# Optimization experiments

Hardware: AMD Instinct MI355X
Metric: run time of the kernel (lower is better)

Reference implementation:

```python
import jax, jax.numpy as jnp
import numpy as np

N, R, A, F = 6000, 5, 8, 128
K, O = 2, 128
RADIUS = 0.028
ROT_DELTA = 1


def _kernel_matrix(n_radial, n_angular, radius):
    # polar grid of kernel vertices -> cartesian, shape (R, A, 2)
    r = radius * (np.arange(1, n_radial + 1, dtype=np.float64) / n_radial)
    theta = 2.0 * np.pi * np.arange(n_angular, dtype=np.float64) / n_angular
    x = r[:, None] * np.cos(theta)[None, :]
    y = r[:, None] * np.sin(theta)[None, :]
    return np.stack([x, y], axis=-1)


def _interp_coefficients(n_radial, n_angular, radius):
    # Gaussian interpolation weights w(rho_a,theta_b,rho_c,theta_d), normalized,
    # reshaped to (R, A, R*A) as in _configure_patch_operator.
    kv = _kernel_matrix(n_radial, n_angular, radius)           # (R, A, 2)
    flat = kv.reshape(-1, 2)                                   # (R*A, 2)
    d2 = ((kv[:, :, None, :] - flat[None, None, :, :]) ** 2).sum(-1)  # (R, A, R*A)
    sigma = radius / n_radial
    w = np.exp(-d2 / (2.0 * sigma * sigma))
    w = w / w.sum(axis=-1, keepdims=True)
    return w.astype(np.float32)


def setup_inputs() -> dict:
    key = jax.random.key(0)
    k1, k2, k3, k4, k5 = jax.random.split(key, 5)
    mesh_signal = jax.random.normal(k1, (N, F), dtype=jnp.float32)
    # barycentric coords: channel 0 = vertex indices (stored as float), channel 1 = weights summing to 1
    idx = jax.random.randint(k2, (N, R, A, 3), 0, N).astype(jnp.float32)
    w = jax.random.uniform(k3, (N, R, A, 3), dtype=jnp.float32)
    w = w / w.sum(axis=-1, keepdims=True)
    bary_coordinates = jnp.stack([idx, w], axis=-1)            # (N, R, A, 3, 2)
    kernel_weights = jax.random.normal(k4, (R, A, K, O, F), dtype=jnp.float32) * 0.05
    bias = jax.random.normal(k5, (K, O), dtype=jnp.float32) * 0.05
    interp_coeffs = jnp.asarray(_interp_coefficients(R, A, RADIUS))  # (R, A, R*A)
    return {"mesh_signal": mesh_signal, "bary_coordinates": bary_coordinates,
            "kernel_weights": kernel_weights, "bias": bias, "interp_coeffs": interp_coeffs}


def reference(mesh_signal, bary_coordinates, kernel_weights, bias, interp_coeffs):
    # 1) gather + barycentric interpolation
    idx = bary_coordinates[..., 0].astype(jnp.int32)           # (N, R, A, 3)
    w = bary_coordinates[..., 1]                               # (N, R, A, 3)
    collected = mesh_signal[idx]                               # (N, R, A, 3, F)
    sig = jnp.sum(w[..., None] * collected, axis=-2)           # (N, R, A, F)
    # 2) patch operator: F_x @ I[a,b]
    flat = sig.reshape(-1, R * A, F)                           # (N, R*A, F)
    patched = jnp.einsum('nqf,raq->nraf', flat, interp_coeffs)  # (N, R, A, F)
    # 3) rotation-shifted fold (splits=1 -> single chunk; splits don't change math)
    outs = []
    for rot in range(0, A, ROT_DELTA):
        rolled = jnp.roll(patched, shift=rot, axis=2)          # (N, R, A, F)
        s = jnp.einsum('nraf,rakof->nko', rolled, kernel_weights) + (R * A) * bias  # (N, K, O)
        outs.append(jax.nn.relu(s).sum(axis=1))                # (N, O)
    return jnp.stack(outs, axis=1)                             # (N, n_rotations, O)
```

## Files before the change

kernel.cpp:

```cpp
#include <hip/hip_runtime.h>
#include <hip/hip_bf16.h>


#define N_PTS 6000
#define RR 5
#define AA 8
#define FF 128
#define OO 128
#define QQ 40
#define KD2 1280
#define SIG_BLOCKS 750
#define W2_BLOCKS 128
#define CCQ 0.70710678118654752f
#define RT2 1.41421356237309515f

#define AHS ((size_t)N_PTS * KD2)
#define BHS ((size_t)512 * KD2)

typedef __bf16 bf16_t;
typedef __bf16 bf16x4 __attribute__((ext_vector_type(4)));
typedef __bf16 bf16x8 __attribute__((ext_vector_type(8)));
typedef float f32x4 __attribute__((ext_vector_type(4)));

#define GLOAD_LDS16(g, l)                                              \
  __builtin_amdgcn_global_load_lds(                                    \
      (const __attribute__((address_space(1))) void*)(g),              \
      (__attribute__((address_space(3))) void*)(l), 16, 0, 0)

#define DFT8V(xx, c, X0, X4, Xr1, Xi1, Xr2, Xi2, Xr3, Xi3)             \
  {                                                                    \
    const float s0_ = xx[0][c] + xx[4][c], s1_ = xx[1][c] + xx[5][c];  \
    const float s2_ = xx[2][c] + xx[6][c], s3_ = xx[3][c] + xx[7][c];  \
    const float d0_ = xx[0][c] - xx[4][c], d1_ = xx[1][c] - xx[5][c];  \
    const float d2_ = xx[2][c] - xx[6][c], d3_ = xx[3][c] - xx[7][c];  \
    const float e_ = CCQ * (d1_ - d3_), o_ = CCQ * (d1_ + d3_);        \
    X0 = (s0_ + s2_) + (s1_ + s3_);                                    \
    X4 = (s0_ + s2_) - (s1_ + s3_);                                    \
    Xr2 = s0_ - s2_; Xi2 = s3_ - s1_;                                  \
    Xr1 = d0_ + e_;  Xi1 = -(o_ + d2_);                                \
    Xr3 = d0_ - e_;  Xi3 = d2_ - o_;                                   \
  }

#define PACK4(dst, X)                                                  \
  {                                                                    \
    bf16x4 pv_;                                                        \
    pv_[0] = (bf16_t)X[0]; pv_[1] = (bf16_t)X[1];                      \
    pv_[2] = (bf16_t)X[2]; pv_[3] = (bf16_t)X[3];                      \
    *(bf16x4*)(dst) = pv_;                                             \
  }

__global__ __launch_bounds__(256) void prep_fft_kernel(
    const float* __restrict__ mesh, const float* __restrict__ bary,
    const float* __restrict__ kw, const float* __restrict__ interp,
    bf16_t* __restrict__ Ahat, bf16_t* __restrict__ Bhat) {
  __shared__ float sI[RR * AA * QQ];
  const int bx = blockIdx.x;
  const int tid = threadIdx.x;

  if (bx < SIG_BLOCKS) {
    const int slot = tid >> 5;
    const int l = tid & 31;
    const int n = bx * 8 + slot;
    const float* bn = bary + (size_t)n * (QQ * 6);
    bf16_t* an = Ahat + (size_t)n * KD2 + l * 4;
#pragma unroll
    for (int rho = 0; rho < RR; ++rho) {
      float x[8][4];
#pragma unroll
      for (int a = 0; a < 8; ++a) {
        const float* b = bn + (rho * 8 + a) * 6;
        const float2 p0 = *(const float2*)(b);
        const float2 p1 = *(const float2*)(b + 2);
        const float2 p2 = *(const float2*)(b + 4);
        const float4 v0 =
            *(const float4*)(mesh + (size_t)((int)p0.x) * FF + l * 4);
        const float4 v1 =
            *(const float4*)(mesh + (size_t)((int)p1.x) * FF + l * 4);
        const float4 v2 =
            *(const float4*)(mesh + (size_t)((int)p2.x) * FF + l * 4);
        x[a][0] = p0.y * v0.x + p1.y * v1.x + p2.y * v2.x;
        x[a][1] = p0.y * v0.y + p1.y * v1.y + p2.y * v2.y;
        x[a][2] = p0.y * v0.z + p1.y * v1.z + p2.y * v2.z;
        x[a][3] = p0.y * v0.w + p1.y * v1.w + p2.y * v2.w;
      }
      float X0[4], X4[4], Xr1[4], Xi1[4], Xr2[4], Xi2[4], Xr3[4], Xi3[4];
#pragma unroll
      for (int c = 0; c < 4; ++c)
        DFT8V(x, c, X0[c], X4[c], Xr1[c], Xi1[c], Xr2[c], Xi2[c], Xr3[c],
              Xi3[c]);
      bf16_t* dst = an + rho * 256;
      PACK4(dst, X0);                  PACK4(dst + 128, X4);
      PACK4(dst + AHS, Xr1);           PACK4(dst + AHS + 128, Xi1);
      PACK4(dst + 2 * AHS, Xr2);       PACK4(dst + 2 * AHS + 128, Xi2);
      PACK4(dst + 3 * AHS, Xr3);       PACK4(dst + 3 * AHS + 128, Xi3);
    }
  } else {
    const int j = (bx - SIG_BLOCKS) * 2 + (tid >> 7);
    const int f = tid & 127;
    for (int i = tid; i < RR * AA * QQ; i += 256) sI[i] = interp[i];
    __syncthreads();
    const int o = (j >> 1) & 127;
    const int k = j & 1;
    float acc[QQ];
#pragma unroll
    for (int q = 0; q < QQ; ++q) acc[q] = 0.f;
    for (int r = 0; r < RR; ++r) {
      for (int a = 0; a < AA; ++a) {
        const float kv =
            kw[((size_t)((r * AA + a) * 2 + k) * OO + o) * FF + f];
        const float4* ip = (const float4*)(sI + (r * AA + a) * QQ);
#pragma unroll
        for (int q4 = 0; q4 < QQ / 4; ++q4) {
          const float4 w4 = ip[q4];
          acc[q4 * 4 + 0] += w4.x * kv;
          acc[q4 * 4 + 1] += w4.y * kv;
          acc[q4 * 4 + 2] += w4.z * kv;
          acc[q4 * 4 + 3] += w4.w * kv;
        }
      }
    }
    const float SC = 0.125f;
    bf16_t* b1p = Bhat + (size_t)j * KD2 + f;
    bf16_t* b2p = Bhat + (size_t)(256 + j) * KD2 + f;
#pragma unroll
    for (int rho = 0; rho < RR; ++rho) {
      float xx[8][1];
#pragma unroll
      for (int a = 0; a < 8; ++a) xx[a][0] = acc[rho * 8 + a];
      float Y0, Y4, Yr1, Yi1, Yr2, Yi2, Yr3, Yi3;
      DFT8V(xx, 0, Y0, Y4, Yr1, Yi1, Yr2, Yi2, Yr3, Yi3);
      const int off = rho * 256;
      b1p[off] = (bf16_t)(Y0 * SC);        b1p[off + 128] = (bf16_t)0.f;
      b2p[off] = (bf16_t)0.f;              b2p[off + 128] = (bf16_t)(Y4 * SC);
      b1p[BHS + off] = (bf16_t)(Yr1 * SC);
      b1p[BHS + off + 128] = (bf16_t)(Yi1 * SC);
      b2p[BHS + off] = (bf16_t)(Yi1 * SC);
      b2p[BHS + off + 128] = (bf16_t)(-Yr1 * SC);
      b1p[2 * BHS + off] = (bf16_t)(Yr2 * SC);
      b1p[2 * BHS + off + 128] = (bf16_t)(Yi2 * SC);
      b2p[2 * BHS + off] = (bf16_t)(Yi2 * SC);
      b2p[2 * BHS + off + 128] = (bf16_t)(-Yr2 * SC);
      b1p[3 * BHS + off] = (bf16_t)(Yr3 * SC);
      b1p[3 * BHS + off + 128] = (bf16_t)(Yi3 * SC);
      b2p[3 * BHS + off] = (bf16_t)(Yi3 * SC);
      b2p[3 * BHS + off + 128] = (bf16_t)(-Yr3 * SC);
    }
  }
}

__global__ __launch_bounds__(256, 3) void gemm_fused_fft_kernel(
    const bf16_t* __restrict__ Ahat, const bf16_t* __restrict__ Bhat,
    const float* __restrict__ bias, float* __restrict__ out) {
  const int L = blockIdx.x;
  const int xcd = L & 7;
  const int t = L >> 3;
  const int g = xcd + 8 * (t >> 4);
  const int jt = t & 15;
  const int m0 = g * 128;
  if (m0 >= N_PTS) return;
  const int j0 = jt * 16;

  __shared__ bf16_t As[128 * 64];
  __shared__ bf16_t Bs[32 * 64];
  const int tid = threadIdx.x;
  const int wave = tid >> 6;
  const int lane = tid & 63;
  const int quad = lane >> 4;
  const int tl = lane & 15;
  const int wm = wave * 32;
  const int srow = lane >> 3;
  const int sc = (lane & 7) ^ srow;

  const int crow = wave * 8;
  const int colbase = (crow < 16) ? (j0 + crow) : (256 + j0 + (crow - 16));
  const int gcol = colbase + srow;

  static const float CF[4][8] = {
      {1, 1, 1, 1, 1, 1, 1, 1},
      {2, RT2, 0, -RT2, -2, -RT2, 0, RT2},
      {2, 0, -2, 0, 2, 0, -2, 0},
      {2, -RT2, 0, RT2, -2, RT2, 0, -RT2}};
  static const float SF[4][8] = {
      {1, -1, 1, -1, 1, -1, 1, -1},
      {0, -RT2, -2, -RT2, 0, RT2, 2, RT2},
      {0, -2, 0, 2, 0, -2, 0, 2},
      {0, -RT2, 2, -RT2, 0, RT2, -2, RT2}};

  f32x4 oacc[8][2];
#pragma unroll
  for (int rot = 0; rot < 8; ++rot)
#pragma unroll
    for (int mm = 0; mm < 2; ++mm) oacc[rot][mm] = {0.f, 0.f, 0.f, 0.f};

#pragma unroll
  for (int b = 0; b < 4; ++b) {
    const bf16_t* A = Ahat + (size_t)b * AHS;
    const bf16_t* B = Bhat + (size_t)b * BHS;
    f32x4 z[2][2];
#pragma unroll
    for (int mm = 0; mm < 2; ++mm)
#pragma unroll
      for (int cc = 0; cc < 2; ++cc) z[mm][cc] = {0.f, 0.f, 0.f, 0.f};

    for (int kk = 0; kk < KD2; kk += 64) {
      __syncthreads();
#pragma unroll
      for (int i = 0; i < 4; ++i) {
        const int row = wave * 32 + i * 8;
        int gm = m0 + row + srow;
        gm = gm < N_PTS ? gm : (N_PTS - 1);
        GLOAD_LDS16(A + (size_t)gm * KD2 + kk + sc * 8, As + row * 64);
      }
      GLOAD_LDS16(B + (size_t)gcol * KD2 + kk + sc * 8, Bs + crow * 64);
      __syncthreads();
#pragma unroll
      for (int ks = 0; ks < 2; ++ks) {
        const int ch = (((ks * 4 + quad) ^ (tl & 7)) * 8);
        bf16x8 af[2], bfr[2];
        af[0] = *(const bf16x8*)(As + (wm + tl) * 64 + ch);
        af[1] = *(const bf16x8*)(As + (wm + 16 + tl) * 64 + ch);
        bfr[0] = *(const bf16x8*)(Bs + tl * 64 + ch);
        bfr[1] = *(const bf16x8*)(Bs + (16 + tl) * 64 + ch);
#pragma unroll
        for (int mm = 0; mm < 2; ++mm)
#pragma unroll
          for (int cc = 0; cc < 2; ++cc)
            z[mm][cc] = __builtin_amdgcn_mfma_f32_16x16x32_bf16(
                af[mm], bfr[cc], z[mm][cc], 0, 0, 0);
      }
    }
#pragma unroll
    for (int rot = 0; rot < 8; ++rot) {
      const float cf = CF[b][rot], sf = SF[b][rot];
#pragma unroll
      for (int mm = 0; mm < 2; ++mm)
#pragma unroll
        for (int r = 0; r < 4; ++r)
          oacc[rot][mm][r] += cf * z[mm][0][r] + sf * z[mm][1][r];
    }
  }

  const int j = j0 + tl;
  const float bb = 40.0f * bias[((j & 1) << 7) | (j >> 1)];
  const int o = j >> 1;
#pragma unroll
  for (int rot = 0; rot < 8; ++rot)
#pragma unroll
    for (int mm = 0; mm < 2; ++mm)
#pragma unroll
      for (int r = 0; r < 4; ++r) {
        const int mrow = m0 + wm + mm * 16 + quad * 4 + r;
        float v = oacc[rot][mm][r] + bb;
        v = v > 0.f ? v : 0.f;
        const float vs = v + __shfl_xor(v, 1, 64);
        if (((lane & 1) == 0) && (mrow < N_PTS))
          out[(size_t)mrow * 1024 + rot * 128 + o] = vs;
      }
}

extern "C" void kernel_launch(void* const* d_in, const int* in_sizes, int n_in,
                              void* d_out, int out_size, void* d_ws,
                              size_t ws_size, hipStream_t stream) {
  const float* mesh = (const float*)d_in[0];
  const float* bary = (const float*)d_in[1];
  const float* kw = (const float*)d_in[2];
  const float* bias = (const float*)d_in[3];
  const float* interp = (const float*)d_in[4];
  float* out = (float*)d_out;

  bf16_t* Ahat = (bf16_t*)d_ws;
  bf16_t* Bhat = (bf16_t*)((char*)d_ws + 4 * AHS * 2);

  prep_fft_kernel<<<SIG_BLOCKS + W2_BLOCKS, 256, 0, stream>>>(
      mesh, bary, kw, interp, Ahat, Bhat);
  gemm_fused_fft_kernel<<<768, 256, 0, stream>>>(Ahat, Bhat, bias, out);
}
```

Baseline: 160.3 us.

## Double-buffer B tiles in LDS and load A fragments directly into registers

Restructures the GEMM main loop into a software pipeline. B tiles are staged through two alternating LDS buffers, and the A operand is loaded straight from global memory into MFMA register fragments instead of going through shared memory. The next tile's loads, including the first tile of the next FFT component, are issued before computing on the current one, which halves the barriers per tile and overlaps memory latency with MFMA work. In exchange it uses more registers for the prefetched A fragments. The A loads also lose coalescing, since each lane now reads 16-byte chunks from separate rows.

Result: slower. 229.4 us (+43.1%).

```diff
diff --git a/kernel.cpp b/kernel.cpp
--- a/kernel.cpp
+++ b/kernel.cpp
@@ -160,8 +160,8 @@
   if (m0 >= N_PTS) return;
   const int j0 = jt * 16;
 
-  __shared__ bf16_t As[128 * 64];
-  __shared__ bf16_t Bs[32 * 64];
+  __shared__ bf16_t Bs0[32 * 64];
+  __shared__ bf16_t Bs1[32 * 64];
   const int tid = threadIdx.x;
   const int wave = tid >> 6;
   const int lane = tid & 63;
@@ -173,7 +173,12 @@
 
   const int crow = wave * 8;
   const int colbase = (crow < 16) ? (j0 + crow) : (256 + j0 + (crow - 16));
-  const int gcol = colbase + srow;
+  const size_t bcol = (size_t)(colbase + srow) * KD2 + sc * 8;
+
+  int r0 = m0 + wm + tl;       r0 = r0 < N_PTS ? r0 : (N_PTS - 1);
+  int r1 = m0 + wm + 16 + tl;  r1 = r1 < N_PTS ? r1 : (N_PTS - 1);
+  const size_t ro0 = (size_t)r0 * KD2 + quad * 8;
+  const size_t ro1 = (size_t)r1 * KD2 + quad * 8;
 
   static const float CF[4][8] = {
       {1, 1, 1, 1, 1, 1, 1, 1},
@@ -192,52 +197,82 @@
 #pragma unroll
     for (int mm = 0; mm < 2; ++mm) oacc[rot][mm] = {0.f, 0.f, 0.f, 0.f};
 
+#define STAGE_B(Bp, kkv, bufn) \
+  GLOAD_LDS16((Bp) + bcol + (kkv), Bs##bufn + crow * 64)
+
+#define LOAD_A(p0, p1, p2, p3, Ap, kkv)                   \
+  p0 = *(const bf16x8*)((Ap) + ro0 + (kkv));              \
+  p1 = *(const bf16x8*)((Ap) + ro1 + (kkv));              \
+  p2 = *(const bf16x8*)((Ap) + ro0 + (kkv) + 32);         \
+  p3 = *(const bf16x8*)((Ap) + ro1 + (kkv) + 32);
+
+#define COMPUTE(Bsx, p0, p1, p2, p3)                                        \
+  {                                                                         \
+    const int ch0 = (quad ^ (tl & 7)) * 8;                                  \
+    const int ch1 = ((4 + quad) ^ (tl & 7)) * 8;                            \
+    bf16x8 b0 = *(const bf16x8*)(Bsx + tl * 64 + ch0);                      \
+    bf16x8 b1 = *(const bf16x8*)(Bsx + (16 + tl) * 64 + ch0);               \
+    z00 = __builtin_amdgcn_mfma_f32_16x16x32_bf16(p0, b0, z00, 0, 0, 0);    \
+    z01 = __builtin_amdgcn_mfma_f32_16x16x32_bf16(p0, b1, z01, 0, 0, 0);    \
+    z10 = __builtin_amdgcn_mfma_f32_16x16x32_bf16(p1, b0, z10, 0, 0, 0);    \
+    z11 = __builtin_amdgcn_mfma_f32_16x16x32_bf16(p1, b1, z11, 0, 0, 0);    \
+    b0 = *(const bf16x8*)(Bsx + tl * 64 + ch1);                             \
+    b1 = *(const bf16x8*)(Bsx + (16 + tl) * 64 + ch1);                      \
+    z00 = __builtin_amdgcn_mfma_f32_16x16x32_bf16(p2, b0, z00, 0, 0, 0);    \
+    z01 = __builtin_amdgcn_mfma_f32_16x16x32_bf16(p2, b1, z01, 0, 0, 0);    \
+    z10 = __builtin_amdgcn_mfma_f32_16x16x32_bf16(p3, b0, z10, 0, 0, 0);    \
+    z11 = __builtin_amdgcn_mfma_f32_16x16x32_bf16(p3, b1, z11, 0, 0, 0);    \
+  }
+
+  bf16x8 aA0, aA1, aA2, aA3, aB0, aB1, aB2, aB3;
+  f32x4 z00, z01, z10, z11;
+
+  const bf16_t* A = Ahat;
+  const bf16_t* B = Bhat;
+  STAGE_B(B, 0, 0);
+  LOAD_A(aA0, aA1, aA2, aA3, A, 0);
+  __syncthreads();
+
 #pragma unroll
   for (int b = 0; b < 4; ++b) {
-    const bf16_t* A = Ahat + (size_t)b * AHS;
-    const bf16_t* B = Bhat + (size_t)b * BHS;
-    f32x4 z[2][2];
-#pragma unroll
-    for (int mm = 0; mm < 2; ++mm)
-#pragma unroll
-      for (int cc = 0; cc < 2; ++cc) z[mm][cc] = {0.f, 0.f, 0.f, 0.f};
-
-    for (int kk = 0; kk < KD2; kk += 64) {
+    z00 = {0.f, 0.f, 0.f, 0.f};
+    z01 = {0.f, 0.f, 0.f, 0.f};
+    z10 = {0.f, 0.f, 0.f, 0.f};
+    z11 = {0.f, 0.f, 0.f, 0.f};
+    int kk = 0;
+#pragma unroll 1
+    for (int d = 0; d < 9; ++d) {
+      STAGE_B(B, kk + 64, 1);
+      LOAD_A(aB0, aB1, aB2, aB3, A, kk + 64);
+      COMPUTE(Bs0, aA0, aA1, aA2, aA3);
       __syncthreads();
-#pragma unroll
-      for (int i = 0; i < 4; ++i) {
-        const int row = wave * 32 + i * 8;
-        int gm = m0 + row + srow;
-        gm = gm < N_PTS ? gm : (N_PTS - 1);
-        GLOAD_LDS16(A + (size_t)gm * KD2 + kk + sc * 8, As + row * 64);
-      }
-      GLOAD_LDS16(B + (size_t)gcol * KD2 + kk + sc * 8, Bs + crow * 64);
+      STAGE_B(B, kk + 128, 0);
+      LOAD_A(aA0, aA1, aA2, aA3, A, kk + 128);
+      COMPUTE(Bs1, aB0, aB1, aB2, aB3);
       __syncthreads();
-#pragma unroll
-      for (int ks = 0; ks < 2; ++ks) {
-        const int ch = (((ks * 4 + quad) ^ (tl & 7)) * 8);
-        bf16x8 af[2], bfr[2];
-        af[0] = *(const bf16x8*)(As + (wm + tl) * 64 + ch);
-        af[1] = *(const bf16x8*)(As + (wm + 16 + tl) * 64 + ch);
-        bfr[0] = *(const bf16x8*)(Bs + tl * 64 + ch);
-        bfr[1] = *(const bf16x8*)(Bs + (16 + tl) * 64 + ch);
-#pragma unroll
-        for (int mm = 0; mm < 2; ++mm)
-#pragma unroll
-          for (int cc = 0; cc < 2; ++cc)
-            z[mm][cc] = __builtin_amdgcn_mfma_f32_16x16x32_bf16(
-                af[mm], bfr[cc], z[mm][cc], 0, 0, 0);
-      }
-    }
+      kk += 128;
+    }
+    STAGE_B(B, 1216, 1);
+    LOAD_A(aB0, aB1, aB2, aB3, A, 1216);
+    COMPUTE(Bs0, aA0, aA1, aA2, aA3);
+    __syncthreads();
+    if (b < 3) {
+      STAGE_B(B + BHS, 0, 0);
+      LOAD_A(aA0, aA1, aA2, aA3, A + AHS, 0);
+    }
+    COMPUTE(Bs1, aB0, aB1, aB2, aB3);
+    __syncthreads();
 #pragma unroll
     for (int rot = 0; rot < 8; ++rot) {
       const float cf = CF[b][rot], sf = SF[b][rot];
 #pragma unroll
-      for (int mm = 0; mm < 2; ++mm)
-#pragma unroll
-        for (int r = 0; r < 4; ++r)
-          oacc[rot][mm][r] += cf * z[mm][0][r] + sf * z[mm][1][r];
-    }
+      for (int r = 0; r < 4; ++r) {
+        oacc[rot][0][r] += cf * z00[r] + sf * z01[r];
+        oacc[rot][1][r] += cf * z10[r] + sf * z11[r];
+      }
+    }
+    A += AHS;
+    B += BHS;
   }
 
   const int j = j0 + tl;
```

## Remap signal gather to one wavefront per point with LDS-staged barycentric records

Applied to the files above, without the earlier changes.

The signal-prep blocks now assign one 64-lane wavefront per mesh point, each lane handling two features, instead of 32 lanes handling four features. This doubles the number of signal blocks and adds occupancy hints to the launch bounds. The barycentric records for the block's four points are staged cooperatively into shared memory rather than read redundantly by every lane from global memory. The aim is more parallelism and fewer redundant global loads for the latency-bound gather, at the cost of narrower 8-byte gathers and stores and an added block barrier.

Result: slower. 241.1 us (+50.4%).

```diff
diff --git a/kernel.cpp b/kernel.cpp
--- a/kernel.cpp
+++ b/kernel.cpp
@@ -9,7 +9,7 @@
 #define OO 128
 #define QQ 40
 #define KD2 1280
-#define SIG_BLOCKS 750
+#define SIG_BLOCKS 1500
 #define W2_BLOCKS 128
 #define CCQ 0.70710678118654752f
 #define RT2 1.41421356237309515f
@@ -18,7 +18,7 @@
 #define BHS ((size_t)512 * KD2)
 
 typedef __bf16 bf16_t;
-typedef __bf16 bf16x4 __attribute__((ext_vector_type(4)));
+typedef __bf16 bf16x2 __attribute__((ext_vector_type(2)));
 typedef __bf16 bf16x8 __attribute__((ext_vector_type(8)));
 typedef float f32x4 __attribute__((ext_vector_type(4)));
 
@@ -41,63 +41,63 @@
     Xr3 = d0_ - e_;  Xi3 = d2_ - o_;                                   \
   }
 
-#define PACK4(dst, X)                                                  \
+#define PACK2(dst, X)                                                  \
   {                                                                    \
-    bf16x4 pv_;                                                        \
+    bf16x2 pv_;                                                        \
     pv_[0] = (bf16_t)X[0]; pv_[1] = (bf16_t)X[1];                      \
-    pv_[2] = (bf16_t)X[2]; pv_[3] = (bf16_t)X[3];                      \
-    *(bf16x4*)(dst) = pv_;                                             \
-  }
-
-__global__ __launch_bounds__(256) void prep_fft_kernel(
+    *(bf16x2*)(dst) = pv_;                                             \
+  }
+
+__global__ __launch_bounds__(256, 6) void prep_fft_kernel(
     const float* __restrict__ mesh, const float* __restrict__ bary,
     const float* __restrict__ kw, const float* __restrict__ interp,
     bf16_t* __restrict__ Ahat, bf16_t* __restrict__ Bhat) {
-  __shared__ float sI[RR * AA * QQ];
+  __shared__ float sh[RR * AA * QQ];
   const int bx = blockIdx.x;
   const int tid = threadIdx.x;
 
   if (bx < SIG_BLOCKS) {
-    const int slot = tid >> 5;
-    const int l = tid & 31;
-    const int n = bx * 8 + slot;
-    const float* bn = bary + (size_t)n * (QQ * 6);
-    bf16_t* an = Ahat + (size_t)n * KD2 + l * 4;
+    const int wave = tid >> 6;
+    const int l = tid & 63;
+    const int n = bx * 4 + wave;
+    const float* bbase = bary + (size_t)bx * 4 * (QQ * 6);
+    for (int i = tid; i < 960; i += 256) sh[i] = bbase[i];
+    __syncthreads();
+    const float* bp = sh + wave * 240;
+    bf16_t* an = Ahat + (size_t)n * KD2 + l * 2;
 #pragma unroll
     for (int rho = 0; rho < RR; ++rho) {
-      float x[8][4];
+      float x[8][2];
 #pragma unroll
       for (int a = 0; a < 8; ++a) {
-        const float* b = bn + (rho * 8 + a) * 6;
-        const float2 p0 = *(const float2*)(b);
-        const float2 p1 = *(const float2*)(b + 2);
-        const float2 p2 = *(const float2*)(b + 4);
-        const float4 v0 =
-            *(const float4*)(mesh + (size_t)((int)p0.x) * FF + l * 4);
-        const float4 v1 =
-            *(const float4*)(mesh + (size_t)((int)p1.x) * FF + l * 4);
-        const float4 v2 =
-            *(const float4*)(mesh + (size_t)((int)p2.x) * FF + l * 4);
+        const float* rec = bp + (rho * 8 + a) * 6;
+        const float2 p0 = *(const float2*)(rec);
+        const float2 p1 = *(const float2*)(rec + 2);
+        const float2 p2 = *(const float2*)(rec + 4);
+        const float2 v0 =
+            *(const float2*)(mesh + (size_t)((int)p0.x) * FF + l * 2);
+        const float2 v1 =
+            *(const float2*)(mesh + (size_t)((int)p1.x) * FF + l * 2);
+        const float2 v2 =
+            *(const float2*)(mesh + (size_t)((int)p2.x) * FF + l * 2);
         x[a][0] = p0.y * v0.x + p1.y * v1.x + p2.y * v2.x;
         x[a][1] = p0.y * v0.y + p1.y * v1.y + p2.y * v2.y;
-        x[a][2] = p0.y * v0.z + p1.y * v1.z + p2.y * v2.z;
-        x[a][3] = p0.y * v0.w + p1.y * v1.w + p2.y * v2.w;
-      }
-      float X0[4], X4[4], Xr1[4], Xi1[4], Xr2[4], Xi2[4], Xr3[4], Xi3[4];
-#pragma unroll
-      for (int c = 0; c < 4; ++c)
+      }
+      float X0[2], X4[2], Xr1[2], Xi1[2], Xr2[2], Xi2[2], Xr3[2], Xi3[2];
+#pragma unroll
+      for (int c = 0; c < 2; ++c)
         DFT8V(x, c, X0[c], X4[c], Xr1[c], Xi1[c], Xr2[c], Xi2[c], Xr3[c],
               Xi3[c]);
       bf16_t* dst = an + rho * 256;
-      PACK4(dst, X0);                  PACK4(dst + 128, X4);
-      PACK4(dst + AHS, Xr1);           PACK4(dst + AHS + 128, Xi1);
-      PACK4(dst + 2 * AHS, Xr2);       PACK4(dst + 2 * AHS + 128, Xi2);
-      PACK4(dst + 3 * AHS, Xr3);       PACK4(dst + 3 * AHS + 128, Xi3);
+      PACK2(dst, X0);                  PACK2(dst + 128, X4);
+      PACK2(dst + AHS, Xr1);           PACK2(dst + AHS + 128, Xi1);
+      PACK2(dst + 2 * AHS, Xr2);       PACK2(dst + 2 * AHS + 128, Xi2);
+      PACK2(dst + 3 * AHS, Xr3);       PACK2(dst + 3 * AHS + 128, Xi3);
     }
   } else {
     const int j = (bx - SIG_BLOCKS) * 2 + (tid >> 7);
     const int f = tid & 127;
-    for (int i = tid; i < RR * AA * QQ; i += 256) sI[i] = interp[i];
+    for (int i = tid; i < RR * AA * QQ; i += 256) sh[i] = interp[i];
     __syncthreads();
     const int o = (j >> 1) & 127;
     const int k = j & 1;
@@ -108,7 +108,7 @@
       for (int a = 0; a < AA; ++a) {
         const float kv =
             kw[((size_t)((r * AA + a) * 2 + k) * OO + o) * FF + f];
-        const float4* ip = (const float4*)(sI + (r * AA + a) * QQ);
+        const float4* ip = (const float4*)(sh + (r * AA + a) * QQ);
 #pragma unroll
         for (int q4 = 0; q4 < QQ / 4; ++q4) {
           const float4 w4 = ip[q4];
```

## Interleave re/im pairs in A/B spectra and stage bary records in LDS

Applied to the files above, without the earlier changes.

Changes the K-dimension layout of Ahat and Bhat so paired spectral components (X0/X4, real/imag) sit next to each other. This allows 16-byte bf16x8 stores in the signal path and bf16x2 stores in the weight path instead of scattered 4-byte and 2-byte writes. The per-block barycentric records are loaded cooperatively into shared memory, and launch bounds request higher occupancy. The GEMM kernel is unchanged, which is only valid if its dot-product reduction is invariant to the consistent K permutation applied to both A and B.

After: 165.6 us. 1.03x slower.

```diff
diff --git a/kernel.cpp b/kernel.cpp
--- a/kernel.cpp
+++ b/kernel.cpp
@@ -18,7 +18,7 @@
 #define BHS ((size_t)512 * KD2)
 
 typedef __bf16 bf16_t;
-typedef __bf16 bf16x4 __attribute__((ext_vector_type(4)));
+typedef __bf16 bf16x2 __attribute__((ext_vector_type(2)));
 typedef __bf16 bf16x8 __attribute__((ext_vector_type(8)));
 typedef float f32x4 __attribute__((ext_vector_type(4)));
 
@@ -41,19 +41,21 @@
     Xr3 = d0_ - e_;  Xi3 = d2_ - o_;                                   \
   }
 
-#define PACK4(dst, X)                                                  \
+#define PACKP(dst, P, Q)                                               \
   {                                                                    \
-    bf16x4 pv_;                                                        \
-    pv_[0] = (bf16_t)X[0]; pv_[1] = (bf16_t)X[1];                      \
-    pv_[2] = (bf16_t)X[2]; pv_[3] = (bf16_t)X[3];                      \
-    *(bf16x4*)(dst) = pv_;                                             \
-  }
-
-__global__ __launch_bounds__(256) void prep_fft_kernel(
+    bf16x8 pv_;                                                        \
+    pv_[0] = (bf16_t)P[0]; pv_[1] = (bf16_t)Q[0];                      \
+    pv_[2] = (bf16_t)P[1]; pv_[3] = (bf16_t)Q[1];                      \
+    pv_[4] = (bf16_t)P[2]; pv_[5] = (bf16_t)Q[2];                      \
+    pv_[6] = (bf16_t)P[3]; pv_[7] = (bf16_t)Q[3];                      \
+    *(bf16x8*)(dst) = pv_;                                             \
+  }
+
+__global__ __launch_bounds__(256, 6) void prep_fft_kernel(
     const float* __restrict__ mesh, const float* __restrict__ bary,
     const float* __restrict__ kw, const float* __restrict__ interp,
     bf16_t* __restrict__ Ahat, bf16_t* __restrict__ Bhat) {
-  __shared__ float sI[RR * AA * QQ];
+  __shared__ float sh[1920];
   const int bx = blockIdx.x;
   const int tid = threadIdx.x;
 
@@ -61,17 +63,20 @@
     const int slot = tid >> 5;
     const int l = tid & 31;
     const int n = bx * 8 + slot;
-    const float* bn = bary + (size_t)n * (QQ * 6);
-    bf16_t* an = Ahat + (size_t)n * KD2 + l * 4;
+    const float* bbase = bary + (size_t)bx * 8 * (QQ * 6);
+    for (int i = tid; i < 1920; i += 256) sh[i] = bbase[i];
+    __syncthreads();
+    const float* bp = sh + slot * 240;
+    bf16_t* an = Ahat + (size_t)n * KD2 + l * 8;
 #pragma unroll
     for (int rho = 0; rho < RR; ++rho) {
       float x[8][4];
 #pragma unroll
       for (int a = 0; a < 8; ++a) {
-        const float* b = bn + (rho * 8 + a) * 6;
-        const float2 p0 = *(const float2*)(b);
-        const float2 p1 = *(const float2*)(b + 2);
-        const float2 p2 = *(const float2*)(b + 4);
+        const float* rec = bp + (rho * 8 + a) * 6;
+        const float2 p0 = *(const float2*)(rec);
+        const float2 p1 = *(const float2*)(rec + 2);
+        const float2 p2 = *(const float2*)(rec + 4);
         const float4 v0 =
             *(const float4*)(mesh + (size_t)((int)p0.x) * FF + l * 4);
         const float4 v1 =
@@ -89,15 +94,15 @@
         DFT8V(x, c, X0[c], X4[c], Xr1[c], Xi1[c], Xr2[c], Xi2[c], Xr3[c],
               Xi3[c]);
       bf16_t* dst = an + rho * 256;
-      PACK4(dst, X0);                  PACK4(dst + 128, X4);
-      PACK4(dst + AHS, Xr1);           PACK4(dst + AHS + 128, Xi1);
-      PACK4(dst + 2 * AHS, Xr2);       PACK4(dst + 2 * AHS + 128, Xi2);
-      PACK4(dst + 3 * AHS, Xr3);       PACK4(dst + 3 * AHS + 128, Xi3);
+      PACKP(dst, X0, X4);
+      PACKP(dst + AHS, Xr1, Xi1);
+      PACKP(dst + 2 * AHS, Xr2, Xi2);
+      PACKP(dst + 3 * AHS, Xr3, Xi3);
     }
   } else {
     const int j = (bx - SIG_BLOCKS) * 2 + (tid >> 7);
     const int f = tid & 127;
-    for (int i = tid; i < RR * AA * QQ; i += 256) sI[i] = interp[i];
+    for (int i = tid; i < RR * AA * QQ; i += 256) sh[i] = interp[i];
     __syncthreads();
     const int o = (j >> 1) & 127;
     const int k = j & 1;
@@ -108,7 +113,7 @@
       for (int a = 0; a < AA; ++a) {
         const float kv =
             kw[((size_t)((r * AA + a) * 2 + k) * OO + o) * FF + f];
-        const float4* ip = (const float4*)(sI + (r * AA + a) * QQ);
+        const float4* ip = (const float4*)(sh + (r * AA + a) * QQ);
 #pragma unroll
         for (int q4 = 0; q4 < QQ / 4; ++q4) {
           const float4 w4 = ip[q4];
@@ -120,8 +125,8 @@
       }
     }
     const float SC = 0.125f;
-    bf16_t* b1p = Bhat + (size_t)j * KD2 + f;
-    bf16_t* b2p = Bhat + (size_t)(256 + j) * KD2 + f;
+    bf16_t* b1p = Bhat + (size_t)j * KD2;
+    bf16_t* b2p = Bhat + (size_t)(256 + j) * KD2;
 #pragma unroll
     for (int rho = 0; rho < RR; ++rho) {
       float xx[8][1];
@@ -129,21 +134,24 @@
       for (int a = 0; a < 8; ++a) xx[a][0] = acc[rho * 8 + a];
       float Y0, Y4, Yr1, Yi1, Yr2, Yi2, Yr3, Yi3;
       DFT8V(xx, 0, Y0, Y4, Yr1, Yi1, Yr2, Yi2, Yr3, Yi3);
-      const int off = rho * 256;
-      b1p[off] = (bf16_t)(Y0 * SC);        b1p[off + 128] = (bf16_t)0.f;
-      b2p[off] = (bf16_t)0.f;              b2p[off + 128] = (bf16_t)(Y4 * SC);
-      b1p[BHS + off] = (bf16_t)(Yr1 * SC);
-      b1p[BHS + off + 128] = (bf16_t)(Yi1 * SC);
-      b2p[BHS + off] = (bf16_t)(Yi1 * SC);
-      b2p[BHS + off + 128] = (bf16_t)(-Yr1 * SC);
-      b1p[2 * BHS + off] = (bf16_t)(Yr2 * SC);
-      b1p[2 * BHS + off + 128] = (bf16_t)(Yi2 * SC);
-      b2p[2 * BHS + off] = (bf16_t)(Yi2 * SC);
-      b2p[2 * BHS + off + 128] = (bf16_t)(-Yr2 * SC);
-      b1p[3 * BHS + off] = (bf16_t)(Yr3 * SC);
-      b1p[3 * BHS + off + 128] = (bf16_t)(Yi3 * SC);
-      b2p[3 * BHS + off] = (bf16_t)(Yi3 * SC);
-      b2p[3 * BHS + off + 128] = (bf16_t)(-Yr3 * SC);
+      const int off = rho * 256 + f * 2;
+      bf16x2 w;
+      w[0] = (bf16_t)(Y0 * SC);   w[1] = (bf16_t)0.f;
+      *(bf16x2*)(b1p + off) = w;
+      w[0] = (bf16_t)0.f;         w[1] = (bf16_t)(Y4 * SC);
+      *(bf16x2*)(b2p + off) = w;
+      w[0] = (bf16_t)(Yr1 * SC);  w[1] = (bf16_t)(Yi1 * SC);
+      *(bf16x2*)(b1p + BHS + off) = w;
+      w[0] = (bf16_t)(Yi1 * SC);  w[1] = (bf16_t)(-Yr1 * SC);
+      *(bf16x2*)(b2p + BHS + off) = w;
+      w[0] = (bf16_t)(Yr2 * SC);  w[1] = (bf16_t)(Yi2 * SC);
+      *(bf16x2*)(b1p + 2 * BHS + off) = w;
+      w[0] = (bf16_t)(Yi2 * SC);  w[1] = (bf16_t)(-Yr2 * SC);
+      *(bf16x2*)(b2p + 2 * BHS + off) = w;
+      w[0] = (bf16_t)(Yr3 * SC);  w[1] = (bf16_t)(Yi3 * SC);
+      *(bf16x2*)(b1p + 3 * BHS + off) = w;
+      w[0] = (bf16_t)(Yi3 * SC);  w[1] = (bf16_t)(-Yr3 * SC);
+      *(bf16x2*)(b2p + 3 * BHS + off) = w;
     }
   }
 }
```
